# Kernel optimization log

Hardware: AMD Instinct MI355X
Metric: run time of the kernel (lower is better)

The kernel has to match this reference:

```python
import jax, jax.numpy as jnp
import numpy as np

EMBED_DIM = 768
NUM_HEADS = 12
HEAD_DIM = EMBED_DIM // NUM_HEADS


def setup_inputs() -> dict:
    key = jax.random.key(0)
    k1, k2, k3, k4, k5 = jax.random.split(key, 5)
    x = jax.random.normal(k1, (2, 4096, EMBED_DIM), dtype=jnp.float32)
    # nn.Linear(embedding_dim, 3*embedding_dim): weight [3d, d], bias [3d]
    w_qkv = jax.random.normal(k2, (3 * EMBED_DIM, EMBED_DIM), dtype=jnp.float32) * (1.0 / np.sqrt(EMBED_DIM))
    b_qkv = jax.random.normal(k3, (3 * EMBED_DIM,), dtype=jnp.float32) * 0.02
    # LayerNorm affine params
    ln_gamma = jnp.ones((EMBED_DIM,), dtype=jnp.float32)
    ln_beta = jnp.zeros((EMBED_DIM,), dtype=jnp.float32)
    return {"x": x, "w_qkv": w_qkv, "b_qkv": b_qkv, "ln_gamma": ln_gamma, "ln_beta": ln_beta}


def _layernorm(x, gamma, beta, eps=1e-5):
    mu = jnp.mean(x, axis=-1, keepdims=True)
    var = jnp.var(x, axis=-1, keepdims=True)
    return (x - mu) * jax.lax.rsqrt(var + eps) * gamma + beta


def reference(x, w_qkv, b_qkv, ln_gamma, ln_beta):
    b, n, d = x.shape
    h, hd = NUM_HEADS, HEAD_DIM
    qkv = x @ w_qkv.T + b_qkv                      # [b, n, 3d]
    qkv = qkv.reshape(b, n, 3, h, hd)
    qkv = jnp.transpose(qkv, (2, 0, 3, 1, 4))      # [3, b, h, n, hd]
    Q, K, V = qkv[0], qkv[1], qkv[2]
    scale = 1.0 / np.sqrt(hd).astype(np.float32)
    scores = jnp.einsum('bhqd,bhkd->bhqk', Q, K) * scale   # [b, h, n, n]
    attn = jax.nn.softmax(scores, axis=-1)
    out = jnp.einsum('bhqk,bhkd->bhqd', attn, V)           # [b, h, n, hd]
    out = jnp.transpose(out, (0, 2, 1, 3)).reshape(b, n, d)
    return _layernorm(x + out, ln_gamma, ln_beta)
```

## Files before the change

kernel.cpp:

```cpp
#include <hip/hip_runtime.h>
#include <stdint.h>

#define NUM_HEADS 12
#define HEAD_DIM 64
#define EMB 768
#define SEQ 4096
#define BATCH 2
#define ROWS (BATCH*SEQ)
#define DQKV (3*EMB)

typedef __attribute__((ext_vector_type(8))) __bf16 bf16x8;
typedef __attribute__((ext_vector_type(4))) float floatx4;

static __device__ __forceinline__ unsigned short f2bf(float f) {
  unsigned int u = __float_as_uint(f);
  u += 0x7FFFu + ((u >> 16) & 1u);
  return (unsigned short)(u >> 16);
}

static __device__ __forceinline__ float bf2f(unsigned short h) {
  return __uint_as_float(((unsigned int)h) << 16);
}

static __device__ __forceinline__ unsigned int pack_bf2_trunc(float a, float b) {
  return __builtin_amdgcn_perm(__float_as_uint(b), __float_as_uint(a), 0x07060302u);
}

static __device__ __forceinline__ void async_cp16(void* lds, const void* g) {
  __builtin_amdgcn_global_load_lds(
      (__attribute__((address_space(1))) void*)(g),
      (__attribute__((address_space(3))) void*)(lds), 16, 0, 0);
}

static __device__ __forceinline__ int perm_key(int nn) {
  return (nn & ~31) | (((nn >> 2) & 3) * 8 + ((nn >> 4) & 1) * 4 + (nn & 3));
}

#define N4X (ROWS*EMB/4)
#define N4W (DQKV*EMB/4)
__global__ __launch_bounds__(256) void cvt2_kernel(
    const float* __restrict__ x, const float* __restrict__ w,
    unsigned short* __restrict__ xb, unsigned short* __restrict__ wb) {
  int i = blockIdx.x * blockDim.x + threadIdx.x;
  const float4* src;
  ushort4* dst;
  if (i < N4X) { src = (const float4*)x; dst = (ushort4*)xb; }
  else { i -= N4X; if (i >= N4W) return; src = (const float4*)w; dst = (ushort4*)wb; }
  float4 v = src[i];
  ushort4 o;
  o.x = f2bf(v.x); o.y = f2bf(v.y); o.z = f2bf(v.z); o.w = f2bf(v.w);
  dst[i] = o;
}

__global__ __launch_bounds__(256) void qkv_gemm_kernel(
    const unsigned short* __restrict__ xb, const unsigned short* __restrict__ wb,
    const float* __restrict__ bias,
    unsigned short* __restrict__ Qb, unsigned short* __restrict__ Kb,
    unsigned short* __restrict__ Vt) {
  __shared__ unsigned short As[128 * 64];
  __shared__ unsigned short Bs[128 * 64];
  const int t = threadIdx.x;
  const int lane = t & 63;
  const int w = t >> 6;
  const int wm = w >> 1, wn = w & 1;
  const int fr = lane & 15, fq = lane >> 4;
  const int fx = fr & 7;
  const int m0 = blockIdx.x * 128;
  const int n0 = blockIdx.y * 128;
  const int sel = n0 / EMB;
  const int lr = t >> 3;
  const int sc = t & 7;

  floatx4 acc[4][4];
#pragma unroll
  for (int i = 0; i < 4; ++i)
#pragma unroll
    for (int j = 0; j < 4; ++j) acc[i][j] = (floatx4)(0.0f);

  if (sel < 2) {
    for (int k0 = 0; k0 < EMB; k0 += 64) {
      __syncthreads();
#pragma unroll
      for (int i = 0; i < 4; ++i) {
        const int rr = i*32 + lr;
        const int cg = ((sc ^ (lr & 7)) * 8);
        async_cp16(&As[rr*64 + sc*8], &xb[(size_t)(m0 + rr)*EMB + k0 + cg]);
        async_cp16(&Bs[rr*64 + sc*8], &wb[(size_t)(n0 + rr)*EMB + k0 + cg]);
      }
      __syncthreads();
#pragma unroll
      for (int ks = 0; ks < 2; ++ks) {
        bf16x8 af[4], bfr[4];
#pragma unroll
        for (int i = 0; i < 4; ++i)
          af[i] = *(const bf16x8*)&As[(wm*64 + i*16 + fr)*64 + (((ks*4+fq) ^ fx)*8)];
#pragma unroll
        for (int j = 0; j < 4; ++j)
          bfr[j] = *(const bf16x8*)&Bs[(wn*64 + j*16 + fr)*64 + (((ks*4+fq) ^ fx)*8)];
#pragma unroll
        for (int i = 0; i < 4; ++i)
#pragma unroll
          for (int j = 0; j < 4; ++j)
            acc[i][j] = __builtin_amdgcn_mfma_f32_16x16x32_bf16(bfr[j], af[i], acc[i][j], 0, 0, 0);
      }
    }
    const float qscale = 0.125f * 1.4426950408889634f;
    const float sc2 = (sel == 0) ? qscale : 1.0f;
    unsigned short* dst = (sel == 0) ? Qb : Kb;
#pragma unroll
    for (int i = 0; i < 4; ++i) {
      const int mr = m0 + wm*64 + i*16 + fr;
      const int b = mr / SEQ;
      const int nn = mr - b*SEQ;
#pragma unroll
      for (int j = 0; j < 4; ++j) {
        const int og = n0 + wn*64 + j*16 + fq*4;
        const int oo = og - sel*EMB;
        const int hh = oo >> 6, dd = oo & 63;
        const float4 bv = *(const float4*)&bias[og];
        ushort4 pk;
        pk.x = f2bf((acc[i][j][0] + bv.x) * sc2);
        pk.y = f2bf((acc[i][j][1] + bv.y) * sc2);
        pk.z = f2bf((acc[i][j][2] + bv.z) * sc2);
        pk.w = f2bf((acc[i][j][3] + bv.w) * sc2);
        *(ushort4*)&dst[(((size_t)(b*NUM_HEADS + hh))*SEQ + nn)*HEAD_DIM + dd] = pk;
      }
    }
  } else {
    for (int k0 = 0; k0 < EMB; k0 += 64) {
      __syncthreads();
#pragma unroll
      for (int i = 0; i < 4; ++i) {
        const int rr = i*32 + lr;
        const int cg = ((sc ^ (lr & 7)) * 8);
        async_cp16(&As[rr*64 + sc*8], &xb[(size_t)(m0 + rr)*EMB + k0 + cg]);
        async_cp16(&Bs[rr*64 + sc*8], &wb[(size_t)(n0 + rr)*EMB + k0 + cg]);
      }
      __syncthreads();
#pragma unroll
      for (int ks = 0; ks < 2; ++ks) {
        bf16x8 af[4], bfr[4];
#pragma unroll
        for (int i = 0; i < 4; ++i)
          af[i] = *(const bf16x8*)&As[(wm*64 + i*16 + fr)*64 + (((ks*4+fq) ^ fx)*8)];
#pragma unroll
        for (int j = 0; j < 4; ++j)
          bfr[j] = *(const bf16x8*)&Bs[(wn*64 + j*16 + fr)*64 + (((ks*4+fq) ^ fx)*8)];
#pragma unroll
        for (int i = 0; i < 4; ++i)
#pragma unroll
          for (int j = 0; j < 4; ++j)
            acc[i][j] = __builtin_amdgcn_mfma_f32_16x16x32_bf16(af[i], bfr[j], acc[i][j], 0, 0, 0);
      }
    }
#pragma unroll
    for (int i = 0; i < 4; ++i) {
      const int mr = m0 + wm*64 + i*16 + fq*4;
      const int b = mr / SEQ;
      const int nn = perm_key(mr - b*SEQ);
#pragma unroll
      for (int j = 0; j < 4; ++j) {
        const int feat = n0 + wn*64 + j*16 + fr;
        const int oo = feat - 2*EMB;
        const int hh = oo >> 6, dd = oo & 63;
        const float bv = bias[feat];
        ushort4 pk;
        pk.x = f2bf(acc[i][j][0] + bv);
        pk.y = f2bf(acc[i][j][1] + bv);
        pk.z = f2bf(acc[i][j][2] + bv);
        pk.w = f2bf(acc[i][j][3] + bv);
        *(ushort4*)&Vt[(((size_t)(b*NUM_HEADS + hh))*HEAD_DIM + dd)*SEQ + nn] = pk;
      }
    }
  }
}

__global__ __launch_bounds__(256, 4) void attn_kernel(
    const unsigned short* __restrict__ Qb, const unsigned short* __restrict__ Kb,
    const unsigned short* __restrict__ Vt, unsigned short* __restrict__ Oo) {
  __shared__ unsigned short Ks[128 * 64];
  __shared__ unsigned short Vs[2][64 * 64];
  const int t = threadIdx.x;
  const int lane = t & 63;
  const int w = t >> 6;
  const int fr = lane & 15, fq = lane >> 4;
  const int fx = fr & 7;
  const int bh = blockIdx.y;
  const int q0 = blockIdx.x * 128 + w * 32;

  bf16x8 aq[2][2];
#pragma unroll
  for (int g = 0; g < 2; ++g) {
    const size_t qoff = ((size_t)bh * SEQ + q0 + g*16 + fr) * HEAD_DIM;
    aq[g][0] = *(const bf16x8*)&Qb[qoff + fq*8];
    aq[g][1] = *(const bf16x8*)&Qb[qoff + 32 + fq*8];
  }

  union { unsigned int u[4]; bf16x8 b; } onesu;
  onesu.u[0] = onesu.u[1] = onesu.u[2] = onesu.u[3] = 0x3F803F80u;
  const bf16x8 onesb = onesu.b;

  floatx4 o[2][4];
  floatx4 lsum[2];
#pragma unroll
  for (int g = 0; g < 2; ++g) {
    lsum[g] = (floatx4)(0.f);
#pragma unroll
    for (int d = 0; d < 4; ++d) o[g][d] = (floatx4)(0.f);
  }

  const size_t kb = (size_t)bh * SEQ * HEAD_DIM;
  const size_t vb = (size_t)bh * HEAD_DIM * SEQ;

  auto sfrag = [&](int J2, floatx4 zz[2][2]) {
#pragma unroll
    for (int jj = 0; jj < 2; ++jj) {
      const int row = (J2*2 + jj)*16 + fr;
      bf16x8 k0 = *(const bf16x8*)&Ks[row*64 + ((fq ^ fx)*8)];
      bf16x8 k1 = *(const bf16x8*)&Ks[row*64 + (((fq+4) ^ fx)*8)];
#pragma unroll
      for (int g = 0; g < 2; ++g) {
        floatx4 a = (floatx4)(0.f);
        a = __builtin_amdgcn_mfma_f32_16x16x32_bf16(k0, aq[g][0], a, 0, 0, 0);
        a = __builtin_amdgcn_mfma_f32_16x16x32_bf16(k1, aq[g][1], a, 0, 0, 0);
        zz[g][jj] = a;
      }
    }
  };

  for (int kc = 0; kc < SEQ; kc += 128) {
    __syncthreads();
#pragma unroll
    for (int i = 0; i < 4; ++i) {
      const int chunk = i*256 + t;
      const int r = chunk >> 3, c = chunk & 7;
      async_cp16(&Ks[chunk*8], &Kb[kb + (size_t)(kc + r)*HEAD_DIM + ((c ^ (r&7))*8)]);
    }
#pragma unroll
    for (int i = 0; i < 4; ++i) {
      const int chunk = i*256 + t;
      const int h = chunk >> 9, rem = chunk & 511;
      const int r = rem >> 3, c = rem & 7;
      async_cp16(&Vs[0][0] + chunk*8,
                 &Vt[vb + (size_t)r*SEQ + kc + h*64 + ((c ^ (r&7))*8)]);
    }
    __syncthreads();

    floatx4 z[2][2];
    sfrag(0, z);
#pragma unroll
    for (int J = 0; J < 4; ++J) {
      floatx4 zn[2][2];
      if (J < 3) sfrag(J+1, zn);
      bf16x8 ap[2];
#pragma unroll
      for (int g = 0; g < 2; ++g) {
        float e0 = __builtin_amdgcn_exp2f(z[g][0][0]);
        float e1 = __builtin_amdgcn_exp2f(z[g][0][1]);
        float e2 = __builtin_amdgcn_exp2f(z[g][0][2]);
        float e3 = __builtin_amdgcn_exp2f(z[g][0][3]);
        float e4 = __builtin_amdgcn_exp2f(z[g][1][0]);
        float e5 = __builtin_amdgcn_exp2f(z[g][1][1]);
        float e6 = __builtin_amdgcn_exp2f(z[g][1][2]);
        float e7 = __builtin_amdgcn_exp2f(z[g][1][3]);
        union { unsigned int u[4]; bf16x8 b; } cv;
        cv.u[0] = pack_bf2_trunc(e0, e1);
        cv.u[1] = pack_bf2_trunc(e2, e3);
        cv.u[2] = pack_bf2_trunc(e4, e5);
        cv.u[3] = pack_bf2_trunc(e6, e7);
        ap[g] = cv.b;
      }
#pragma unroll
      for (int g = 0; g < 2; ++g)
        lsum[g] = __builtin_amdgcn_mfma_f32_16x16x32_bf16(ap[g], onesb, lsum[g], 0, 0, 0);
      const unsigned short* vsh = &Vs[J >> 1][0];
      const int vc = ((4*(J & 1) + fq) ^ fx) * 8;
#pragma unroll
      for (int dt = 0; dt < 4; ++dt) {
        const bf16x8 vvb = *(const bf16x8*)&vsh[(dt*16 + fr)*64 + vc];
#pragma unroll
        for (int g = 0; g < 2; ++g)
          o[g][dt] = __builtin_amdgcn_mfma_f32_16x16x32_bf16(ap[g], vvb, o[g][dt], 0, 0, 0);
      }
      if (J < 3) {
#pragma unroll
        for (int g = 0; g < 2; ++g)
#pragma unroll
          for (int jj = 0; jj < 2; ++jj) z[g][jj] = zn[g][jj];
      }
    }
  }

  const int b = bh / NUM_HEADS, hh = bh - b*NUM_HEADS;
#pragma unroll
  for (int g = 0; g < 2; ++g)
#pragma unroll
    for (int r4 = 0; r4 < 4; ++r4) {
      const float li = 1.0f / lsum[g][r4];
      const size_t obase = ((size_t)b*SEQ + q0 + g*16 + fq*4 + r4)*EMB + hh*HEAD_DIM;
#pragma unroll
      for (int dt = 0; dt < 4; ++dt)
        Oo[obase + dt*16 + fr] = f2bf(o[g][dt][r4] * li);
    }
}

__global__ __launch_bounds__(256) void ln_kernel(
    const float* __restrict__ x, const unsigned short* __restrict__ att,
    const float* __restrict__ gamma, const float* __restrict__ beta,
    float* __restrict__ out) {
  const int row = blockIdx.x * 4 + (threadIdx.x >> 6);
  const int lane = threadIdx.x & 63;
  const size_t base = (size_t)row * EMB;
  float4 v[3];
  float s = 0.f, s2 = 0.f;
#pragma unroll
  for (int k = 0; k < 3; ++k) {
    const int c = lane*4 + k*256;
    const float4 xv = *(const float4*)&x[base + c];
    const ushort4 a4 = *(const ushort4*)&att[base + c];
    v[k].x = xv.x + bf2f(a4.x);
    v[k].y = xv.y + bf2f(a4.y);
    v[k].z = xv.z + bf2f(a4.z);
    v[k].w = xv.w + bf2f(a4.w);
    s  += (v[k].x + v[k].y) + (v[k].z + v[k].w);
    s2 += (v[k].x*v[k].x + v[k].y*v[k].y) + (v[k].z*v[k].z + v[k].w*v[k].w);
  }
#pragma unroll
  for (int off = 1; off < 64; off <<= 1) {
    s  += __shfl_xor(s,  off);
    s2 += __shfl_xor(s2, off);
  }
  const float mean = s * (1.0f / EMB);
  const float var  = s2 * (1.0f / EMB) - mean * mean;
  const float rstd = rsqrtf(var + 1e-5f);
#pragma unroll
  for (int k = 0; k < 3; ++k) {
    const int c = lane*4 + k*256;
    const float4 g4 = *(const float4*)&gamma[c];
    const float4 b4 = *(const float4*)&beta[c];
    float4 ov;
    ov.x = (v[k].x - mean) * rstd * g4.x + b4.x;
    ov.y = (v[k].y - mean) * rstd * g4.y + b4.y;
    ov.z = (v[k].z - mean) * rstd * g4.z + b4.z;
    ov.w = (v[k].w - mean) * rstd * g4.w + b4.w;
    *(float4*)&out[base + c] = ov;
  }
}

extern "C" void kernel_launch(void* const* d_in, const int* in_sizes, int n_in,
                              void* d_out, int out_size, void* d_ws, size_t ws_size,
                              hipStream_t stream) {
  const float* x      = (const float*)d_in[0];
  const float* w_qkv  = (const float*)d_in[1];
  const float* b_qkv  = (const float*)d_in[2];
  const float* gamma  = (const float*)d_in[3];
  const float* beta   = (const float*)d_in[4];
  float* out = (float*)d_out;

  unsigned short* xb = (unsigned short*)d_ws;
  unsigned short* wb = xb + (size_t)ROWS * EMB;
  unsigned short* Qb = wb + (size_t)DQKV * EMB;
  unsigned short* Kb = Qb + (size_t)ROWS * EMB;
  unsigned short* Vt = Kb + (size_t)ROWS * EMB;
  unsigned short* att = Vt + (size_t)ROWS * EMB;

  cvt2_kernel<<<(N4X + N4W + 255)/256, 256, 0, stream>>>(x, w_qkv, xb, wb);
  qkv_gemm_kernel<<<dim3(ROWS/128, DQKV/128), 256, 0, stream>>>(xb, wb, b_qkv, Qb, Kb, Vt);
  attn_kernel<<<dim3(SEQ/128, BATCH*NUM_HEADS), 256, 0, stream>>>(Qb, Kb, Vt, att);
  ln_kernel<<<ROWS/4, 256, 0, stream>>>(x, att, gamma, beta, out);
}
```

Measured before the change: 248.6 us.

## Double-buffer K/V tiles in attention with async prefetch and MFMA priority

Restructures the attention key loop from a single 128-key tile loaded then consumed behind two full barriers into 64-key tiles double-buffered in shared memory. The tile two steps ahead is prefetched while the current one is computed, with explicit vmcnt waits and raw s_barrier in place of __syncthreads. s_setprio is raised around the PV MFMA block to favour matrix issue across waves. In exchange, each step covers half as many keys, so there are more barriers per key, and correctness now depends on hand-counted vmcnt values matching the number of async copies issued.

```diff
diff --git a/kernel.cpp b/kernel.cpp
--- a/kernel.cpp
+++ b/kernel.cpp
@@ -175,10 +175,11 @@
   }
 }
 
+#define NT (SEQ/64)
 __global__ __launch_bounds__(256, 4) void attn_kernel(
     const unsigned short* __restrict__ Qb, const unsigned short* __restrict__ Kb,
     const unsigned short* __restrict__ Vt, unsigned short* __restrict__ Oo) {
-  __shared__ unsigned short Ks[128 * 64];
+  __shared__ unsigned short Ks[2][64 * 64];
   __shared__ unsigned short Vs[2][64 * 64];
   const int t = threadIdx.x;
   const int lane = t & 63;
@@ -212,12 +213,27 @@
   const size_t kb = (size_t)bh * SEQ * HEAD_DIM;
   const size_t vb = (size_t)bh * HEAD_DIM * SEQ;
 
-  auto sfrag = [&](int J2, floatx4 zz[2][2]) {
+  auto stage = [&](int kc, int bi) {
+#pragma unroll
+    for (int i = 0; i < 2; ++i) {
+      const int chunk = i*256 + t;
+      const int r = chunk >> 3, c = chunk & 7;
+      async_cp16(&Ks[bi][chunk*8], &Kb[kb + (size_t)(kc + r)*HEAD_DIM + ((c ^ (r&7))*8)]);
+    }
+#pragma unroll
+    for (int i = 0; i < 2; ++i) {
+      const int chunk = i*256 + t;
+      const int r = chunk >> 3, c = chunk & 7;
+      async_cp16(&Vs[bi][chunk*8], &Vt[vb + (size_t)r*SEQ + kc + ((c ^ (r&7))*8)]);
+    }
+  };
+
+  auto sfrag = [&](const unsigned short* ksp, int J2, floatx4 (&zz)[2][2]) {
 #pragma unroll
     for (int jj = 0; jj < 2; ++jj) {
       const int row = (J2*2 + jj)*16 + fr;
-      bf16x8 k0 = *(const bf16x8*)&Ks[row*64 + ((fq ^ fx)*8)];
-      bf16x8 k1 = *(const bf16x8*)&Ks[row*64 + (((fq+4) ^ fx)*8)];
+      bf16x8 k0 = *(const bf16x8*)&ksp[row*64 + ((fq ^ fx)*8)];
+      bf16x8 k1 = *(const bf16x8*)&ksp[row*64 + (((fq+4) ^ fx)*8)];
 #pragma unroll
       for (int g = 0; g < 2; ++g) {
         floatx4 a = (floatx4)(0.f);
@@ -228,67 +244,64 @@
     }
   };
 
-  for (int kc = 0; kc < SEQ; kc += 128) {
-    __syncthreads();
-#pragma unroll
-    for (int i = 0; i < 4; ++i) {
-      const int chunk = i*256 + t;
-      const int r = chunk >> 3, c = chunk & 7;
-      async_cp16(&Ks[chunk*8], &Kb[kb + (size_t)(kc + r)*HEAD_DIM + ((c ^ (r&7))*8)]);
-    }
-#pragma unroll
-    for (int i = 0; i < 4; ++i) {
-      const int chunk = i*256 + t;
-      const int h = chunk >> 9, rem = chunk & 511;
-      const int r = rem >> 3, c = rem & 7;
-      async_cp16(&Vs[0][0] + chunk*8,
-                 &Vt[vb + (size_t)r*SEQ + kc + h*64 + ((c ^ (r&7))*8)]);
-    }
-    __syncthreads();
-
-    floatx4 z[2][2];
-    sfrag(0, z);
-#pragma unroll
-    for (int J = 0; J < 4; ++J) {
-      floatx4 zn[2][2];
-      if (J < 3) sfrag(J+1, zn);
-      bf16x8 ap[2];
-#pragma unroll
-      for (int g = 0; g < 2; ++g) {
-        float e0 = __builtin_amdgcn_exp2f(z[g][0][0]);
-        float e1 = __builtin_amdgcn_exp2f(z[g][0][1]);
-        float e2 = __builtin_amdgcn_exp2f(z[g][0][2]);
-        float e3 = __builtin_amdgcn_exp2f(z[g][0][3]);
-        float e4 = __builtin_amdgcn_exp2f(z[g][1][0]);
-        float e5 = __builtin_amdgcn_exp2f(z[g][1][1]);
-        float e6 = __builtin_amdgcn_exp2f(z[g][1][2]);
-        float e7 = __builtin_amdgcn_exp2f(z[g][1][3]);
-        union { unsigned int u[4]; bf16x8 b; } cv;
-        cv.u[0] = pack_bf2_trunc(e0, e1);
-        cv.u[1] = pack_bf2_trunc(e2, e3);
-        cv.u[2] = pack_bf2_trunc(e4, e5);
-        cv.u[3] = pack_bf2_trunc(e6, e7);
-        ap[g] = cv.b;
-      }
+  auto softmax_pv = [&](const unsigned short* vsp, int J, floatx4 (&zc)[2][2]) {
+    bf16x8 ap[2];
+#pragma unroll
+    for (int g = 0; g < 2; ++g) {
+      float e0 = __builtin_amdgcn_exp2f(zc[g][0][0]);
+      float e1 = __builtin_amdgcn_exp2f(zc[g][0][1]);
+      float e2 = __builtin_amdgcn_exp2f(zc[g][0][2]);
+      float e3 = __builtin_amdgcn_exp2f(zc[g][0][3]);
+      float e4 = __builtin_amdgcn_exp2f(zc[g][1][0]);
+      float e5 = __builtin_amdgcn_exp2f(zc[g][1][1]);
+      float e6 = __builtin_amdgcn_exp2f(zc[g][1][2]);
+      float e7 = __builtin_amdgcn_exp2f(zc[g][1][3]);
+      union { unsigned int u[4]; bf16x8 b; } cv;
+      cv.u[0] = pack_bf2_trunc(e0, e1);
+      cv.u[1] = pack_bf2_trunc(e2, e3);
+      cv.u[2] = pack_bf2_trunc(e4, e5);
+      cv.u[3] = pack_bf2_trunc(e6, e7);
+      ap[g] = cv.b;
+    }
+    __builtin_amdgcn_s_setprio(1);
+#pragma unroll
+    for (int g = 0; g < 2; ++g)
+      lsum[g] = __builtin_amdgcn_mfma_f32_16x16x32_bf16(ap[g], onesb, lsum[g], 0, 0, 0);
+    const int vc = ((4*J + fq) ^ fx) * 8;
+#pragma unroll
+    for (int dt = 0; dt < 4; ++dt) {
+      const bf16x8 vvb = *(const bf16x8*)&vsp[(dt*16 + fr)*64 + vc];
 #pragma unroll
       for (int g = 0; g < 2; ++g)
-        lsum[g] = __builtin_amdgcn_mfma_f32_16x16x32_bf16(ap[g], onesb, lsum[g], 0, 0, 0);
-      const unsigned short* vsh = &Vs[J >> 1][0];
-      const int vc = ((4*(J & 1) + fq) ^ fx) * 8;
-#pragma unroll
-      for (int dt = 0; dt < 4; ++dt) {
-        const bf16x8 vvb = *(const bf16x8*)&vsh[(dt*16 + fr)*64 + vc];
-#pragma unroll
-        for (int g = 0; g < 2; ++g)
-          o[g][dt] = __builtin_amdgcn_mfma_f32_16x16x32_bf16(ap[g], vvb, o[g][dt], 0, 0, 0);
-      }
-      if (J < 3) {
-#pragma unroll
-        for (int g = 0; g < 2; ++g)
-#pragma unroll
-          for (int jj = 0; jj < 2; ++jj) z[g][jj] = zn[g][jj];
-      }
-    }
+        o[g][dt] = __builtin_amdgcn_mfma_f32_16x16x32_bf16(ap[g], vvb, o[g][dt], 0, 0, 0);
+    }
+    __builtin_amdgcn_s_setprio(0);
+  };
+
+  stage(0, 0);
+  stage(64, 1);
+  asm volatile("s_waitcnt vmcnt(4)" ::: "memory");
+  __builtin_amdgcn_s_barrier();
+
+  int cur = 0;
+  for (int tt = 0; tt < NT; ++tt) {
+    const unsigned short* ksp = Ks[cur];
+    const unsigned short* vsp = Vs[cur];
+    floatx4 z[2][2], zn[2][2];
+    sfrag(ksp, 0, z);
+    sfrag(ksp, 1, zn);
+    softmax_pv(vsp, 0, z);
+    softmax_pv(vsp, 1, zn);
+    if (tt == NT - 1) break;
+    __builtin_amdgcn_s_barrier();
+    if (tt + 2 < NT) {
+      stage((tt + 2) * 64, cur);
+      asm volatile("s_waitcnt vmcnt(4)" ::: "memory");
+    } else {
+      asm volatile("s_waitcnt vmcnt(0)" ::: "memory");
+    }
+    __builtin_amdgcn_s_barrier();
+    cur ^= 1;
   }
 
   const int b = bh / NUM_HEADS, hh = bh - b*NUM_HEADS;
```

Measured after the change: 252.7 us. Within noise of the previous version (+1.6%).

## Split attention key range into two halves and merge partials in layernorm

Applied to the files above, without the earlier changes.

The attention grid gains a z dimension of 2, and each block processes half of the key sequence. Each block writes unnormalized fp32 output partials and row sums to the workspace. The layernorm kernel adds the two partials, divides by the combined sum, and then applies the residual add and normalization. The goal is to raise block count and fill the GPU better, which the original grid of 768 blocks with up to 4 per CU did not do. The cost is extra fp32 partial-buffer traffic and possibly a partial last wave.

```diff
diff --git a/kernel.cpp b/kernel.cpp
--- a/kernel.cpp
+++ b/kernel.cpp
@@ -175,9 +175,11 @@
   }
 }
 
+#define NKH (SEQ/2)
 __global__ __launch_bounds__(256, 4) void attn_kernel(
     const unsigned short* __restrict__ Qb, const unsigned short* __restrict__ Kb,
-    const unsigned short* __restrict__ Vt, unsigned short* __restrict__ Oo) {
+    const unsigned short* __restrict__ Vt,
+    float* __restrict__ Opart, float* __restrict__ lpart) {
   __shared__ unsigned short Ks[128 * 64];
   __shared__ unsigned short Vs[2][64 * 64];
   const int t = threadIdx.x;
@@ -186,6 +188,8 @@
   const int fr = lane & 15, fq = lane >> 4;
   const int fx = fr & 7;
   const int bh = blockIdx.y;
+  const int half = blockIdx.z;
+  const int kc0 = half * NKH;
   const int q0 = blockIdx.x * 128 + w * 32;
 
   bf16x8 aq[2][2];
@@ -212,7 +216,7 @@
   const size_t kb = (size_t)bh * SEQ * HEAD_DIM;
   const size_t vb = (size_t)bh * HEAD_DIM * SEQ;
 
-  auto sfrag = [&](int J2, floatx4 zz[2][2]) {
+  auto sfrag = [&](int J2, floatx4 (&zz)[2][2]) {
 #pragma unroll
     for (int jj = 0; jj < 2; ++jj) {
       const int row = (J2*2 + jj)*16 + fr;
@@ -228,7 +232,7 @@
     }
   };
 
-  for (int kc = 0; kc < SEQ; kc += 128) {
+  for (int kc = kc0; kc < kc0 + NKH; kc += 128) {
     __syncthreads();
 #pragma unroll
     for (int i = 0; i < 4; ++i) {
@@ -291,37 +295,51 @@
     }
   }
 
-  const int b = bh / NUM_HEADS, hh = bh - b*NUM_HEADS;
-#pragma unroll
-  for (int g = 0; g < 2; ++g)
+  const size_t pb = (size_t)(half * BATCH * NUM_HEADS + bh);
+  const size_t obase = pb * SEQ * HEAD_DIM;
+  const size_t lbase = pb * SEQ;
+#pragma unroll
+  for (int g = 0; g < 2; ++g) {
 #pragma unroll
     for (int r4 = 0; r4 < 4; ++r4) {
-      const float li = 1.0f / lsum[g][r4];
-      const size_t obase = ((size_t)b*SEQ + q0 + g*16 + fq*4 + r4)*EMB + hh*HEAD_DIM;
+      const int q = q0 + g*16 + fq*4 + r4;
+      float* op = &Opart[obase + (size_t)q * HEAD_DIM];
 #pragma unroll
       for (int dt = 0; dt < 4; ++dt)
-        Oo[obase + dt*16 + fr] = f2bf(o[g][dt][r4] * li);
-    }
+        op[dt*16 + fr] = o[g][dt][r4];
+      if (fr == 0) lpart[lbase + q] = lsum[g][r4];
+    }
+  }
 }
 
 __global__ __launch_bounds__(256) void ln_kernel(
-    const float* __restrict__ x, const unsigned short* __restrict__ att,
+    const float* __restrict__ x,
+    const float* __restrict__ Opart, const float* __restrict__ lpart,
     const float* __restrict__ gamma, const float* __restrict__ beta,
     float* __restrict__ out) {
   const int row = blockIdx.x * 4 + (threadIdx.x >> 6);
   const int lane = threadIdx.x & 63;
+  const int b = row >> 12;
+  const int n = row & (SEQ - 1);
   const size_t base = (size_t)row * EMB;
+  const size_t HSTRIDE = (size_t)BATCH * NUM_HEADS * SEQ;
+  const size_t HOSTRIDE = HSTRIDE * HEAD_DIM;
   float4 v[3];
   float s = 0.f, s2 = 0.f;
 #pragma unroll
   for (int k = 0; k < 3; ++k) {
     const int c = lane*4 + k*256;
+    const int h = c >> 6, d4 = c & 63;
+    const size_t oi = (((size_t)(b*NUM_HEADS + h))*SEQ + n)*HEAD_DIM + d4;
+    const size_t li = ((size_t)(b*NUM_HEADS + h))*SEQ + n;
+    const float4 p0 = *(const float4*)&Opart[oi];
+    const float4 p1 = *(const float4*)&Opart[oi + HOSTRIDE];
+    const float rl = 1.0f / (lpart[li] + lpart[li + HSTRIDE]);
     const float4 xv = *(const float4*)&x[base + c];
-    const ushort4 a4 = *(const ushort4*)&att[base + c];
-    v[k].x = xv.x + bf2f(a4.x);
-    v[k].y = xv.y + bf2f(a4.y);
-    v[k].z = xv.z + bf2f(a4.z);
-    v[k].w = xv.w + bf2f(a4.w);
+    v[k].x = xv.x + (p0.x + p1.x) * rl;
+    v[k].y = xv.y + (p0.y + p1.y) * rl;
+    v[k].z = xv.z + (p0.z + p1.z) * rl;
+    v[k].w = xv.w + (p0.w + p1.w) * rl;
     s  += (v[k].x + v[k].y) + (v[k].z + v[k].w);
     s2 += (v[k].x*v[k].x + v[k].y*v[k].y) + (v[k].z*v[k].z + v[k].w*v[k].w);
   }
@@ -362,10 +380,11 @@
   unsigned short* Qb = wb + (size_t)DQKV * EMB;
   unsigned short* Kb = Qb + (size_t)ROWS * EMB;
   unsigned short* Vt = Kb + (size_t)ROWS * EMB;
-  unsigned short* att = Vt + (size_t)ROWS * EMB;
+  float* Opart = (float*)(Vt + (size_t)ROWS * EMB);
+  float* lpart = Opart + (size_t)2 * ROWS * EMB;
 
   cvt2_kernel<<<(N4X + N4W + 255)/256, 256, 0, stream>>>(x, w_qkv, xb, wb);
   qkv_gemm_kernel<<<dim3(ROWS/128, DQKV/128), 256, 0, stream>>>(xb, wb, b_qkv, Qb, Kb, Vt);
-  attn_kernel<<<dim3(SEQ/128, BATCH*NUM_HEADS), 256, 0, stream>>>(Qb, Kb, Vt, att);
-  ln_kernel<<<ROWS/4, 256, 0, stream>>>(x, att, gamma, beta, out);
-}
+  attn_kernel<<<dim3(SEQ/128, BATCH*NUM_HEADS, 2), 256, 0, stream>>>(Qb, Kb, Vt, Opart, lpart);
+  ln_kernel<<<ROWS/4, 256, 0, stream>>>(x, Opart, lpart, gamma, beta, out);
+}
```

New measurement: 249.3 us. Within noise of the previous version (+0.3%).

## Widen QKV GEMM tile to 128x256 with swizzled block order and merged loop

Applied to the files above, without the earlier changes.

The QKV projection GEMM now computes 128x256 output tiles per block, so each wave holds a 4x8 set of MFMA accumulators and more B reuse is taken from each A fragment. Block indices are remapped so that groups of 8 consecutive blocks cover different row tiles of the same weight column tile, aiming for better L2 reuse. The two duplicated K loops for Q/K and V are merged into one, with the selection branch placed inside. This doubles B shared memory and accumulator registers, which may cut occupancy, and halves the grid to 576 blocks.

```diff
diff --git a/kernel.cpp b/kernel.cpp
--- a/kernel.cpp
+++ b/kernel.cpp
@@ -58,52 +58,66 @@
     unsigned short* __restrict__ Qb, unsigned short* __restrict__ Kb,
     unsigned short* __restrict__ Vt) {
   __shared__ unsigned short As[128 * 64];
-  __shared__ unsigned short Bs[128 * 64];
+  __shared__ unsigned short Bs[256 * 64];
   const int t = threadIdx.x;
   const int lane = t & 63;
   const int w = t >> 6;
   const int wm = w >> 1, wn = w & 1;
   const int fr = lane & 15, fq = lane >> 4;
   const int fx = fr & 7;
-  const int m0 = blockIdx.x * 128;
-  const int n0 = blockIdx.y * 128;
+  const int orig = blockIdx.x + blockIdx.y * 64;
+  const int r8 = orig >> 3;
+  const int m0 = ((orig & 7) * 8 + (r8 & 7)) * 128;
+  const int n0 = (r8 >> 3) * 256;
   const int sel = n0 / EMB;
-  const int lr = t >> 3;
-  const int sc = t & 7;
-
-  floatx4 acc[4][4];
+
+  floatx4 acc[4][8];
 #pragma unroll
   for (int i = 0; i < 4; ++i)
 #pragma unroll
-    for (int j = 0; j < 4; ++j) acc[i][j] = (floatx4)(0.0f);
+    for (int j = 0; j < 8; ++j) acc[i][j] = (floatx4)(0.0f);
+
+  for (int k0 = 0; k0 < EMB; k0 += 64) {
+    __syncthreads();
+#pragma unroll
+    for (int i = 0; i < 4; ++i) {
+      const int chunk = i*256 + t;
+      const int rr = chunk >> 3, c = chunk & 7;
+      async_cp16(&As[chunk*8], &xb[(size_t)(m0 + rr)*EMB + k0 + ((c ^ (rr&7))*8)]);
+    }
+#pragma unroll
+    for (int i = 0; i < 8; ++i) {
+      const int chunk = i*256 + t;
+      const int rr = chunk >> 3, c = chunk & 7;
+      async_cp16(&Bs[chunk*8], &wb[(size_t)(n0 + rr)*EMB + k0 + ((c ^ (rr&7))*8)]);
+    }
+    __syncthreads();
+#pragma unroll
+    for (int ks = 0; ks < 2; ++ks) {
+      bf16x8 af[4], bfr[8];
+#pragma unroll
+      for (int i = 0; i < 4; ++i)
+        af[i] = *(const bf16x8*)&As[(wm*64 + i*16 + fr)*64 + (((ks*4+fq) ^ fx)*8)];
+#pragma unroll
+      for (int j = 0; j < 8; ++j)
+        bfr[j] = *(const bf16x8*)&Bs[(wn*128 + j*16 + fr)*64 + (((ks*4+fq) ^ fx)*8)];
+      if (sel < 2) {
+#pragma unroll
+        for (int i = 0; i < 4; ++i)
+#pragma unroll
+          for (int j = 0; j < 8; ++j)
+            acc[i][j] = __builtin_amdgcn_mfma_f32_16x16x32_bf16(bfr[j], af[i], acc[i][j], 0, 0, 0);
+      } else {
+#pragma unroll
+        for (int i = 0; i < 4; ++i)
+#pragma unroll
+          for (int j = 0; j < 8; ++j)
+            acc[i][j] = __builtin_amdgcn_mfma_f32_16x16x32_bf16(af[i], bfr[j], acc[i][j], 0, 0, 0);
+      }
+    }
+  }
 
   if (sel < 2) {
-    for (int k0 = 0; k0 < EMB; k0 += 64) {
-      __syncthreads();
-#pragma unroll
-      for (int i = 0; i < 4; ++i) {
-        const int rr = i*32 + lr;
-        const int cg = ((sc ^ (lr & 7)) * 8);
-        async_cp16(&As[rr*64 + sc*8], &xb[(size_t)(m0 + rr)*EMB + k0 + cg]);
-        async_cp16(&Bs[rr*64 + sc*8], &wb[(size_t)(n0 + rr)*EMB + k0 + cg]);
-      }
-      __syncthreads();
-#pragma unroll
-      for (int ks = 0; ks < 2; ++ks) {
-        bf16x8 af[4], bfr[4];
-#pragma unroll
-        for (int i = 0; i < 4; ++i)
-          af[i] = *(const bf16x8*)&As[(wm*64 + i*16 + fr)*64 + (((ks*4+fq) ^ fx)*8)];
-#pragma unroll
-        for (int j = 0; j < 4; ++j)
-          bfr[j] = *(const bf16x8*)&Bs[(wn*64 + j*16 + fr)*64 + (((ks*4+fq) ^ fx)*8)];
-#pragma unroll
-        for (int i = 0; i < 4; ++i)
-#pragma unroll
-          for (int j = 0; j < 4; ++j)
-            acc[i][j] = __builtin_amdgcn_mfma_f32_16x16x32_bf16(bfr[j], af[i], acc[i][j], 0, 0, 0);
-      }
-    }
     const float qscale = 0.125f * 1.4426950408889634f;
     const float sc2 = (sel == 0) ? qscale : 1.0f;
     unsigned short* dst = (sel == 0) ? Qb : Kb;
@@ -113,8 +127,8 @@
       const int b = mr / SEQ;
       const int nn = mr - b*SEQ;
 #pragma unroll
-      for (int j = 0; j < 4; ++j) {
-        const int og = n0 + wn*64 + j*16 + fq*4;
+      for (int j = 0; j < 8; ++j) {
+        const int og = n0 + wn*128 + j*16 + fq*4;
         const int oo = og - sel*EMB;
         const int hh = oo >> 6, dd = oo & 63;
         const float4 bv = *(const float4*)&bias[og];
@@ -127,40 +141,14 @@
       }
     }
   } else {
-    for (int k0 = 0; k0 < EMB; k0 += 64) {
-      __syncthreads();
-#pragma unroll
-      for (int i = 0; i < 4; ++i) {
-        const int rr = i*32 + lr;
-        const int cg = ((sc ^ (lr & 7)) * 8);
-        async_cp16(&As[rr*64 + sc*8], &xb[(size_t)(m0 + rr)*EMB + k0 + cg]);
-        async_cp16(&Bs[rr*64 + sc*8], &wb[(size_t)(n0 + rr)*EMB + k0 + cg]);
-      }
-      __syncthreads();
-#pragma unroll
-      for (int ks = 0; ks < 2; ++ks) {
-        bf16x8 af[4], bfr[4];
-#pragma unroll
-        for (int i = 0; i < 4; ++i)
-          af[i] = *(const bf16x8*)&As[(wm*64 + i*16 + fr)*64 + (((ks*4+fq) ^ fx)*8)];
-#pragma unroll
-        for (int j = 0; j < 4; ++j)
-          bfr[j] = *(const bf16x8*)&Bs[(wn*64 + j*16 + fr)*64 + (((ks*4+fq) ^ fx)*8)];
-#pragma unroll
-        for (int i = 0; i < 4; ++i)
-#pragma unroll
-          for (int j = 0; j < 4; ++j)
-            acc[i][j] = __builtin_amdgcn_mfma_f32_16x16x32_bf16(af[i], bfr[j], acc[i][j], 0, 0, 0);
-      }
-    }
 #pragma unroll
     for (int i = 0; i < 4; ++i) {
       const int mr = m0 + wm*64 + i*16 + fq*4;
       const int b = mr / SEQ;
       const int nn = perm_key(mr - b*SEQ);
 #pragma unroll
-      for (int j = 0; j < 4; ++j) {
-        const int feat = n0 + wn*64 + j*16 + fr;
+      for (int j = 0; j < 8; ++j) {
+        const int feat = n0 + wn*128 + j*16 + fr;
         const int oo = feat - 2*EMB;
         const int hh = oo >> 6, dd = oo & 63;
         const float bv = bias[feat];
@@ -212,7 +200,7 @@
   const size_t kb = (size_t)bh * SEQ * HEAD_DIM;
   const size_t vb = (size_t)bh * HEAD_DIM * SEQ;
 
-  auto sfrag = [&](int J2, floatx4 zz[2][2]) {
+  auto sfrag = [&](int J2, floatx4 (&zz)[2][2]) {
 #pragma unroll
     for (int jj = 0; jj < 2; ++jj) {
       const int row = (J2*2 + jj)*16 + fr;
@@ -365,7 +353,7 @@
   unsigned short* att = Vt + (size_t)ROWS * EMB;
 
   cvt2_kernel<<<(N4X + N4W + 255)/256, 256, 0, stream>>>(x, w_qkv, xb, wb);
-  qkv_gemm_kernel<<<dim3(ROWS/128, DQKV/128), 256, 0, stream>>>(xb, wb, b_qkv, Qb, Kb, Vt);
+  qkv_gemm_kernel<<<dim3(64, 9), 256, 0, stream>>>(xb, wb, b_qkv, Qb, Kb, Vt);
   attn_kernel<<<dim3(SEQ/128, BATCH*NUM_HEADS), 256, 0, stream>>>(Qb, Kb, Vt, att);
   ln_kernel<<<ROWS/4, 256, 0, stream>>>(x, att, gamma, beta, out);
 }
```

Result: slower. 264.2 us (+6.2%).
